# Kernel optimization log

Measured on AMD Instinct MI355X. Metric: run time of the kernel, lower is better.

## Reference

```python
import jax, jax.numpy as jnp
import numpy as np

BS, NQ, NK = 2, 2048, 2048
D_OUT, H, D_K, D_V = 1024, 16, 64, 64


def _xavier(key, shape):
    fan_in, fan_out = shape[1], shape[0]
    lim = float(np.sqrt(6.0 / (fan_in + fan_out)))
    return jax.random.uniform(key, shape, jnp.float32, -lim, lim)


def setup_inputs() -> dict:
    key = jax.random.key(0)
    ks = jax.random.split(key, 9)
    return {
        "queries": jax.random.normal(ks[0], (BS, NQ, D_OUT), jnp.float32),
        "keys": jax.random.normal(ks[1], (BS, NK, D_OUT), jnp.float32),
        "values": jax.random.normal(ks[2], (BS, NK, D_OUT), jnp.float32),
        "mask": jax.random.randint(ks[3], (BS, H, NQ, NK), 0, 2).astype(bool),
        "weights": jax.random.uniform(ks[4], (BS, H, NQ, NK), jnp.float32),
        "Wq": _xavier(ks[5], (H * D_K, D_OUT)),
        "bq": jnp.zeros((H * D_K,), jnp.float32),
        "Wk": _xavier(ks[6], (H * D_K, D_OUT)),
        "bk": jnp.zeros((H * D_K,), jnp.float32),
        "Wv": _xavier(ks[7], (H * D_V, D_OUT)),
        "bv": jnp.zeros((H * D_V,), jnp.float32),
        "Wo": _xavier(ks[8], (D_OUT, H * D_V)),
        "bo": jnp.zeros((D_OUT,), jnp.float32),
    }


def reference(queries, keys, values, mask, weights, Wq, bq, Wk, bk, Wv, bv, Wo, bo):
    bs, nq, _ = queries.shape
    nk = keys.shape[1]
    # projections: (bs, n, h*d) -> (bs, h, n, d)
    q = (queries @ Wq.T + bq).reshape(bs, nq, H, D_K).transpose(0, 2, 1, 3)
    k = (keys @ Wk.T + bk).reshape(bs, nk, H, D_K).transpose(0, 2, 1, 3)
    v = (values @ Wv.T + bv).reshape(bs, nk, H, D_V).transpose(0, 2, 1, 3)
    # scaled dot-product scores: (bs, h, nq, nk)
    att = jnp.einsum("bhqd,bhkd->bhqk", q, k) / jnp.sqrt(jnp.float32(D_K))
    att = att * weights                      # elementwise weight bias
    att = jnp.where(mask, -jnp.inf, att)     # masked_fill(mask, -inf)
    att = jax.nn.softmax(att, axis=-1)
    # dropout is identity at p=0 / eval
    out = jnp.einsum("bhqk,bhkd->bhqd", att, v)  # (bs, h, nq, d_v)
    out = out.transpose(0, 2, 1, 3).reshape(bs, nq, H * D_V)
    return out @ Wo.T + bo
```

## Files before the change

kernel.cpp:

```cpp
#include <hip/hip_runtime.h>
#include <stdint.h>

#define DEV __device__ __forceinline__

typedef __attribute__((__ext_vector_type__(8))) short short8;
typedef __attribute__((__ext_vector_type__(4))) float f32x4;
typedef __attribute__((__ext_vector_type__(16))) float f32x16;
typedef __attribute__((__ext_vector_type__(4))) unsigned short ushort4_t;
typedef __attribute__((__ext_vector_type__(4))) _Float16 half4;
typedef __attribute__((__ext_vector_type__(8))) _Float16 half8;

DEV unsigned short f2bf(float f) {
  union { float f; unsigned u; } x; x.f = f;
  unsigned u = x.u;
  unsigned r = (u + 0x7FFFu + ((u >> 16) & 1u)) >> 16;
  return (unsigned short)r;
}

DEV unsigned short f2h(float f) {
  _Float16 h = (_Float16)f;
  unsigned short u;
  __builtin_memcpy(&u, &h, 2);
  return u;
}

DEV void gload_lds16(const void* g, void* l) {
  __builtin_amdgcn_global_load_lds(
      (const __attribute__((address_space(1))) unsigned int*)g,
      (__attribute__((address_space(3))) unsigned int*)l,
      16, 0, 0);
}

DEV short8 ld_g8(const unsigned short* p) { return *(const short8*)p; }
DEV short8 ld_s8(const unsigned short* p) { return *(const short8*)p; }
DEV half4 ld_h4(const unsigned short* p) {
  half4 r; __builtin_memcpy(&r, p, 8); return r;
}

__global__ void detect_mask_fmt(const unsigned int* __restrict__ mask, int* __restrict__ flag) {
  if (threadIdx.x == 0 && blockIdx.x == 0) {
    int fmt = 1;
    for (int i = 0; i < 256; ++i) {
      unsigned u = mask[i];
      if (u == 0x3F800000u) { fmt = 2; break; }
      if ((u & 0xFFFFFF00u) != 0u) { fmt = 0; break; }
    }
    *flag = fmt;
  }
}

__global__ void pack_mask(const unsigned char* __restrict__ m8,
                          const unsigned int* __restrict__ m32,
                          const int* __restrict__ mfmt,
                          unsigned int* __restrict__ pm) {
  __shared__ unsigned int tile[32 * 65];
  const int bh = blockIdx.x >> 6;
  const int q0 = (blockIdx.x & 63) * 32;
  const int fmt = *mfmt;
  const int tid = threadIdx.x;
#pragma unroll
  for (int rnd = 0; rnd < 8; ++rnd) {
    int w = tid + rnd * 256;
    int q = w >> 6, t = w & 63;
    size_t sb = ((size_t)(bh * 2048 + q0 + q)) * 2048 + t * 32;
    unsigned bits = 0;
    if (fmt == 0) {
      uint4 a = *(const uint4*)(m8 + sb);
      uint4 bq = *(const uint4*)(m8 + sb + 16);
      unsigned wa0 = a.x, wa1 = a.y, wa2 = a.z, wa3 = a.w;
      unsigned wb0 = bq.x, wb1 = bq.y, wb2 = bq.z, wb3 = bq.w;
#pragma unroll
      for (int e = 0; e < 4; ++e) {
        bits |= (((wa0 >> (8 * e)) & 0xFFu) ? 1u : 0u) << (0 + e);
        bits |= (((wa1 >> (8 * e)) & 0xFFu) ? 1u : 0u) << (4 + e);
        bits |= (((wa2 >> (8 * e)) & 0xFFu) ? 1u : 0u) << (8 + e);
        bits |= (((wa3 >> (8 * e)) & 0xFFu) ? 1u : 0u) << (12 + e);
        bits |= (((wb0 >> (8 * e)) & 0xFFu) ? 1u : 0u) << (16 + e);
        bits |= (((wb1 >> (8 * e)) & 0xFFu) ? 1u : 0u) << (20 + e);
        bits |= (((wb2 >> (8 * e)) & 0xFFu) ? 1u : 0u) << (24 + e);
        bits |= (((wb3 >> (8 * e)) & 0xFFu) ? 1u : 0u) << (28 + e);
      }
    } else {
#pragma unroll
      for (int c = 0; c < 8; ++c) {
        uint4 v = *(const uint4*)(m32 + sb + c * 4);
        bits |= (v.x ? 1u : 0u) << (c * 4);
        bits |= (v.y ? 1u : 0u) << (c * 4 + 1);
        bits |= (v.z ? 1u : 0u) << (c * 4 + 2);
        bits |= (v.w ? 1u : 0u) << (c * 4 + 3);
      }
    }
    tile[q * 65 + t] = bits;
  }
  __syncthreads();
#pragma unroll
  for (int rnd = 0; rnd < 8; ++rnd) {
    int w = tid + rnd * 256;
    int t = w >> 5, q = w & 31;
    pm[((size_t)bh * 64 + t) * 2048 + q0 + q] = tile[q * 65 + t];
  }
}

__global__ void cvt_all(const float* __restrict__ q, const float* __restrict__ k,
                        const float* __restrict__ v,
                        const float* __restrict__ wq, const float* __restrict__ wk,
                        const float* __restrict__ wv, const float* __restrict__ wo,
                        unsigned short* __restrict__ Xq, unsigned short* __restrict__ Xk,
                        unsigned short* __restrict__ Xv, unsigned short* __restrict__ Wqb,
                        unsigned short* __restrict__ Wkb, unsigned short* __restrict__ Wvb,
                        unsigned short* __restrict__ Wob) {
  int i = blockIdx.x * 256 + threadIdx.x;
  const float* src; unsigned short* dst; int off;
  if (i < 1048576)      { src = q;  dst = Xq;  off = i; }
  else if (i < 2097152) { src = k;  dst = Xk;  off = i - 1048576; }
  else if (i < 3145728) { src = v;  dst = Xv;  off = i - 2097152; }
  else if (i < 3407872) { src = wq; dst = Wqb; off = i - 3145728; }
  else if (i < 3670016) { src = wk; dst = Wkb; off = i - 3407872; }
  else if (i < 3932160) { src = wv; dst = Wvb; off = i - 3670016; }
  else                  { src = wo; dst = Wob; off = i - 3932160; }
  float4 vv = ((const float4*)src)[off];
  ushort4_t r;
  r.x = f2bf(vv.x); r.y = f2bf(vv.y); r.z = f2bf(vv.z); r.w = f2bf(vv.w);
  ((ushort4_t*)dst)[off] = r;
}

__global__ __launch_bounds__(256, 2) void proj_gemm(
    const unsigned short* __restrict__ Xq, const unsigned short* __restrict__ Xk,
    const unsigned short* __restrict__ Xv,
    const unsigned short* __restrict__ Wqb, const unsigned short* __restrict__ Wkb,
    const unsigned short* __restrict__ Wvb,
    const float* __restrict__ bq, const float* __restrict__ bk, const float* __restrict__ bv,
    unsigned short* __restrict__ QP, unsigned short* __restrict__ KP,
    unsigned short* __restrict__ VT) {
  const int tid = threadIdx.x;
  const int wid = tid >> 6, lane = tid & 63;
  const int l16 = lane & 15, hi = lane >> 4;
  const int m0 = blockIdx.x * 128;
  const int sel = blockIdx.y >> 3;
  const int n0 = (blockIdx.y & 7) * 128;

  const unsigned short* X; const unsigned short* W; const float* bias; unsigned short* out;
  if (sel == 0)      { X = Xq; W = Wqb; bias = bq; out = QP; }
  else if (sel == 1) { X = Xk; W = Wkb; bias = bk; out = KP; }
  else               { X = Xv; W = Wvb; bias = bv; out = VT; }

  __shared__ unsigned short stage[2 * 128 * 32];

  f32x4 acc[4][4] = {};
  const int wm = (wid >> 1) * 64, wn = (wid & 1) * 64;
  const int aoff = (sel == 2) ? 4096 : 0;
  const int boff = 4096 - aoff;

  for (int kt = 0; kt < 1024; kt += 32) {
#pragma unroll
    for (int t = 0; t < 4; ++t) {
      int g = wid * 4 + t;
      int c = g & 7;
      int row = c * 16 + (lane >> 2);
      int ko = (lane & 3) * 8;
      const unsigned short* src = (g < 8)
          ? (X + (size_t)(m0 + row) * 1024 + kt + ko)
          : (W + (size_t)(n0 + row) * 1024 + kt + ko);
      gload_lds16(src, (unsigned short*)((char*)stage + g * 1024));
    }
    __syncthreads();

    short8 af[4], bfr[4];
#pragma unroll
    for (int i = 0; i < 4; ++i)
      af[i] = ld_s8(&stage[aoff + (wm + i * 16 + l16) * 32 + hi * 8]);
#pragma unroll
    for (int j = 0; j < 4; ++j)
      bfr[j] = ld_s8(&stage[boff + (wn + j * 16 + l16) * 32 + hi * 8]);
#pragma unroll
    for (int i = 0; i < 4; ++i)
#pragma unroll
      for (int j = 0; j < 4; ++j)
        acc[i][j] = __builtin_amdgcn_mfma_f32_16x16x32_bf16(af[i], bfr[j], acc[i][j], 0, 0, 0);
    __syncthreads();
  }

  if (sel != 2) {
#pragma unroll
    for (int j = 0; j < 4; ++j) {
      int feat = n0 + wn + j * 16 + l16;
      float bi = bias[feat];
      int h = feat >> 6, d = feat & 63;
#pragma unroll
      for (int i = 0; i < 4; ++i) {
#pragma unroll
        for (int r = 0; r < 4; ++r) {
          int m = m0 + wm + i * 16 + hi * 4 + r;
          int b = m >> 11, n = m & 2047;
          float v = acc[i][j][r] + bi;
          out[(((size_t)(b * 16 + h)) * 2048 + n) * 64 + d] = f2bf(v);
        }
      }
    }
  } else {
#pragma unroll
    for (int j = 0; j < 4; ++j) {
      int tc0 = m0 + wn + j * 16;
      int b = tc0 >> 11, n = tc0 & 2047;
#pragma unroll
      for (int i = 0; i < 4; ++i) {
#pragma unroll
        for (int r = 0; r < 4; ++r) {
          int feat = n0 + wm + i * 16 + hi * 4 + r;
          int h = feat >> 6, d = feat & 63;
          float v = acc[i][j][r] + bias[feat];
          out[((size_t)(b * 16 + h) * 64 + d) * 2048 + n + l16] = f2h(v);
        }
      }
    }
  }
}

__global__ __launch_bounds__(256, 2) void attn_kernel(
    const unsigned short* __restrict__ Q, const unsigned short* __restrict__ K,
    const unsigned short* __restrict__ VT,
    const float* __restrict__ weights,
    const unsigned int* __restrict__ pm,
    unsigned short* __restrict__ O) {
  const int bid = blockIdx.x;
  const int qt = bid >> 5, bh = bid & 31;
  const int b = bh >> 4, h = bh & 15;
  const int tid = threadIdx.x, wid = tid >> 6, lane = tid & 63;
  const int l31 = lane & 31, hh = lane >> 5;
  const size_t bh_nd = (size_t)bh * 2048 * 64;
  const int q0 = qt * 128;
  const int qg = q0 + wid * 32 + l31;

  short8 qf0 = ld_g8(Q + bh_nd + (size_t)qg * 64 + 0  + hh * 8);
  short8 qf1 = ld_g8(Q + bh_nd + (size_t)qg * 64 + 16 + hh * 8);
  short8 qf2 = ld_g8(Q + bh_nd + (size_t)qg * 64 + 32 + hh * 8);
  short8 qf3 = ld_g8(Q + bh_nd + (size_t)qg * 64 + 48 + hh * 8);

  __shared__ float wlds[4][128 * 32];
  __shared__ unsigned short vlds[4][64 * 32];

  const float* wsrc = weights + (size_t)bh * 2048 * 2048;
  const unsigned short* vsrc = VT + bh_nd;
  const unsigned short* ksrc = K + bh_nd;
  const unsigned int* pmsrc = pm + (size_t)bh * 64 * 2048 + qg;
  const int wswz = 4 * ((lane & 7) ^ (lane >> 3));
  const int vswz = 8 * ((lane & 3) ^ ((lane >> 3) & 3));
  const int wrow_s = q0 + wid * 32 + (lane >> 3);
  const int vrow_s = wid * 16 + (lane >> 2);

#define STAGE(BUF, KT)                                                        \
  {                                                                           \
    _Pragma("unroll")                                                         \
    for (int i_ = 0; i_ < 4; ++i_)                                            \
      gload_lds16(wsrc + (size_t)(wrow_s + i_ * 8) * 2048 + (KT) + wswz,      \
                  &wlds[BUF][(wid * 4 + i_) * 256]);                          \
    gload_lds16(vsrc + (size_t)vrow_s * 2048 + (KT) + vswz,                   \
                &vlds[BUF][wid * 512]);                                       \
  }

#define LOADK(K0, K1, K2, K3, PM, T)                                          \
  {                                                                           \
    const int kt_ = (T) * 32;                                                 \
    K0 = ld_g8(ksrc + (size_t)(kt_ + l31) * 64 + 0  + hh * 8);                \
    K1 = ld_g8(ksrc + (size_t)(kt_ + l31) * 64 + 16 + hh * 8);                \
    K2 = ld_g8(ksrc + (size_t)(kt_ + l31) * 64 + 32 + hh * 8);                \
    K3 = ld_g8(ksrc + (size_t)(kt_ + l31) * 64 + 48 + hh * 8);                \
    PM = pmsrc[(size_t)(T) * 2048];                                           \
  }

  f32x16 o0 = {}, o1 = {};
  float mrow = -1e30f, lrow = 0.f;
  short8 ka0, ka1, ka2, ka3, kb0, kb1, kb2, kb3;
  unsigned pma, pmb;

  STAGE(0, 0)
  LOADK(ka0, ka1, ka2, ka3, pma, 0)
  STAGE(1, 32)

#define ITER(T, KC0, KC1, KC2, KC3, PMC, KN0, KN1, KN2, KN3, PMN)             \
  {                                                                           \
    const int t1_ = ((T) + 1) & 63, t2_ = ((T) + 2) & 63;                     \
    LOADK(KN0, KN1, KN2, KN3, PMN, t1_)                                       \
    __builtin_amdgcn_sched_barrier(0);                                        \
    STAGE(((T) + 2) & 3, t2_ * 32)                                            \
    __builtin_amdgcn_sched_barrier(0);                                        \
    asm volatile("s_waitcnt vmcnt(15)" ::: "memory");                         \
    __builtin_amdgcn_s_barrier();                                             \
    __builtin_amdgcn_sched_barrier(0);                                        \
    const int cur_ = (T) & 3;                                                 \
                                                              \
    f32x16 s = {};                                                            \
    s = __builtin_amdgcn_mfma_f32_32x32x16_bf16(KC0, qf0, s, 0, 0, 0);        \
    s = __builtin_amdgcn_mfma_f32_32x32x16_bf16(KC1, qf1, s, 0, 0, 0);        \
    s = __builtin_amdgcn_mfma_f32_32x32x16_bf16(KC2, qf2, s, 0, 0, 0);        \
    s = __builtin_amdgcn_mfma_f32_32x32x16_bf16(KC3, qf3, s, 0, 0, 0);        \
                                                          \
    const float* wrow_ = &wlds[cur_][(wid * 32 + l31) * 32];                  \
    f32x4 wv_[4];                                                             \
    wv_[0] = *(const f32x4*)&wrow_[4 * ((hh + 0) ^ (l31 & 7))];               \
    wv_[1] = *(const f32x4*)&wrow_[4 * ((hh + 2) ^ (l31 & 7))];               \
    wv_[2] = *(const f32x4*)&wrow_[4 * ((hh + 4) ^ (l31 & 7))];               \
    wv_[3] = *(const f32x4*)&wrow_[4 * ((hh + 6) ^ (l31 & 7))];               \
    unsigned mb_ = (PMC) >> (4 * hh);                                         \
    _Pragma("unroll")                                                         \
    for (int r = 0; r < 16; ++r) {                                            \
      bool mk = (mb_ >> ((r & 3) + 8 * (r >> 2))) & 1;                        \
      s[r] = mk ? -INFINITY : s[r] * 0.125f * wv_[r >> 2][r & 3];             \
    }                                                                         \
                                                          \
    float tm = s[0];                                                          \
    _Pragma("unroll")                                                         \
    for (int r = 1; r < 16; ++r) tm = fmaxf(tm, s[r]);                        \
    float tm2 = fmaxf(tm, __shfl_xor(tm, 32));                                \
    if (__any(tm2 > mrow)) {                                                  \
      float mnew = fmaxf(mrow, tm2);                                          \
      float sc = __expf(mrow - mnew);                                         \
      lrow *= sc;                                                             \
      o0 *= sc;                                                               \
      o1 *= sc;                                                               \
      mrow = mnew;                                                            \
    }                                                                         \
    float ps = 0.f;                                                           \
    _Pragma("unroll")                                                         \
    for (int r = 0; r < 16; ++r) {                                            \
      s[r] = __expf(s[r] - mrow);                                             \
      ps += s[r];                                                             \
    }                                                                         \
    lrow += ps;                                                               \
                                                             \
    half8 pa0, pa1;                                                           \
    _Pragma("unroll")                                                         \
    for (int r = 0; r < 8; ++r) {                                             \
      pa0[r] = (_Float16)s[r];                                                \
      pa1[r] = (_Float16)s[8 + r];                                            \
    }                                                                         \
                                                                      \
    {                                                                         \
      const unsigned short* vr_ = &vlds[cur_][l31 * 32];                      \
      half4 a0 = ld_h4(&vr_[4 * ((hh + 0) ^ (l31 & 6))]);                     \
      half4 a1 = ld_h4(&vr_[4 * ((hh + 2) ^ (l31 & 6))]);                     \
      half8 vf;                                                               \
      _Pragma("unroll")                                                       \
      for (int e = 0; e < 4; ++e) { vf[e] = a0[e]; vf[4 + e] = a1[e]; }       \
      o0 = __builtin_amdgcn_mfma_f32_32x32x16_f16(vf, pa0, o0, 0, 0, 0);      \
      half4 b0 = ld_h4(&vr_[4 * ((hh + 4) ^ (l31 & 6))]);                     \
      half4 b1 = ld_h4(&vr_[4 * ((hh + 6) ^ (l31 & 6))]);                     \
      _Pragma("unroll")                                                       \
      for (int e = 0; e < 4; ++e) { vf[e] = b0[e]; vf[4 + e] = b1[e]; }       \
      o0 = __builtin_amdgcn_mfma_f32_32x32x16_f16(vf, pa1, o0, 0, 0, 0);      \
    }                                                                         \
    {                                                                         \
      const unsigned short* vr_ = &vlds[cur_][(32 + l31) * 32];               \
      half4 a0 = ld_h4(&vr_[4 * ((hh + 0) ^ (l31 & 6))]);                     \
      half4 a1 = ld_h4(&vr_[4 * ((hh + 2) ^ (l31 & 6))]);                     \
      half8 vf;                                                               \
      _Pragma("unroll")                                                       \
      for (int e = 0; e < 4; ++e) { vf[e] = a0[e]; vf[4 + e] = a1[e]; }       \
      o1 = __builtin_amdgcn_mfma_f32_32x32x16_f16(vf, pa0, o1, 0, 0, 0);      \
      half4 b0 = ld_h4(&vr_[4 * ((hh + 4) ^ (l31 & 6))]);                     \
      half4 b1 = ld_h4(&vr_[4 * ((hh + 6) ^ (l31 & 6))]);                     \
      _Pragma("unroll")                                                       \
      for (int e = 0; e < 4; ++e) { vf[e] = b0[e]; vf[4 + e] = b1[e]; }       \
      o1 = __builtin_amdgcn_mfma_f32_32x32x16_f16(vf, pa1, o1, 0, 0, 0);      \
    }                                                                         \
  }

  for (int t = 0; t < 64; t += 2) {
    ITER(t,     ka0, ka1, ka2, ka3, pma, kb0, kb1, kb2, kb3, pmb)
    ITER(t + 1, kb0, kb1, kb2, kb3, pmb, ka0, ka1, ka2, ka3, pma)
  }

  lrow += __shfl_xor(lrow, 32);
  float inv = 1.0f / lrow;
  const size_t ob = (size_t)(b * 2048 + qg) * 1024 + h * 64;
#pragma unroll
  for (int j = 0; j < 4; ++j) {
    ushort4_t pk;
    pk.x = f2bf(o0[4 * j + 0] * inv); pk.y = f2bf(o0[4 * j + 1] * inv);
    pk.z = f2bf(o0[4 * j + 2] * inv); pk.w = f2bf(o0[4 * j + 3] * inv);
    *(ushort4_t*)&O[ob + 8 * j + 4 * hh] = pk;
    ushort4_t pk1;
    pk1.x = f2bf(o1[4 * j + 0] * inv); pk1.y = f2bf(o1[4 * j + 1] * inv);
    pk1.z = f2bf(o1[4 * j + 2] * inv); pk1.w = f2bf(o1[4 * j + 3] * inv);
    *(ushort4_t*)&O[ob + 32 + 8 * j + 4 * hh] = pk1;
  }
#undef ITER
#undef LOADK
#undef STAGE
}

__global__ __launch_bounds__(256, 2) void out_gemm(
    const unsigned short* __restrict__ A, const unsigned short* __restrict__ W,
    const float* __restrict__ bias, float* __restrict__ Cout) {
  const int tid = threadIdx.x;
  const int wid = tid >> 6, lane = tid & 63;
  const int l16 = lane & 15, hi = lane >> 4;
  const int m0 = blockIdx.x * 128;
  const int n0 = blockIdx.y * 128;

  __shared__ unsigned short stage[2 * 128 * 32];
  f32x4 acc[4][4] = {};
  const int wm = (wid >> 1) * 64, wn = (wid & 1) * 64;

  for (int kt = 0; kt < 1024; kt += 32) {
#pragma unroll
    for (int t = 0; t < 4; ++t) {
      int g = wid * 4 + t;
      int c = g & 7;
      int row = c * 16 + (lane >> 2);
      int ko = (lane & 3) * 8;
      const unsigned short* src = (g < 8)
          ? (A + (size_t)(m0 + row) * 1024 + kt + ko)
          : (W + (size_t)(n0 + row) * 1024 + kt + ko);
      gload_lds16(src, (unsigned short*)((char*)stage + g * 1024));
    }
    __syncthreads();

    short8 af[4], bfr[4];
#pragma unroll
    for (int i = 0; i < 4; ++i)
      af[i] = ld_s8(&stage[(wm + i * 16 + l16) * 32 + hi * 8]);
#pragma unroll
    for (int j = 0; j < 4; ++j)
      bfr[j] = ld_s8(&stage[4096 + (wn + j * 16 + l16) * 32 + hi * 8]);
#pragma unroll
    for (int i = 0; i < 4; ++i)
#pragma unroll
      for (int j = 0; j < 4; ++j)
        acc[i][j] = __builtin_amdgcn_mfma_f32_16x16x32_bf16(af[i], bfr[j], acc[i][j], 0, 0, 0);
    __syncthreads();
  }

#pragma unroll
  for (int j = 0; j < 4; ++j) {
    int feat = n0 + wn + j * 16 + l16;
    float bi = bias[feat];
#pragma unroll
    for (int i = 0; i < 4; ++i) {
#pragma unroll
      for (int r = 0; r < 4; ++r) {
        int m = m0 + wm + i * 16 + hi * 4 + r;
        Cout[(size_t)m * 1024 + feat] = acc[i][j][r] + bi;
      }
    }
  }
}

extern "C" void kernel_launch(void* const* d_in, const int* in_sizes, int n_in,
                              void* d_out, int out_size, void* d_ws, size_t ws_size,
                              hipStream_t stream) {
  const float* queries = (const float*)d_in[0];
  const float* keys    = (const float*)d_in[1];
  const float* values  = (const float*)d_in[2];
  const void*  maskp   = d_in[3];
  const float* weights = (const float*)d_in[4];
  const float* Wq = (const float*)d_in[5];
  const float* bq = (const float*)d_in[6];
  const float* Wk = (const float*)d_in[7];
  const float* bk = (const float*)d_in[8];
  const float* Wv = (const float*)d_in[9];
  const float* bv = (const float*)d_in[10];
  const float* Wo = (const float*)d_in[11];
  const float* bo = (const float*)d_in[12];

  unsigned short* ws = (unsigned short*)d_ws;
  unsigned short* Xq  = ws;
  unsigned short* Xk  = ws + 4194304;
  unsigned short* Xv  = ws + 8388608;
  unsigned short* Wqb = ws + 12582912;
  unsigned short* Wkb = ws + 13631488;
  unsigned short* Wvb = ws + 14680064;
  unsigned short* Wob = ws + 15728640;
  unsigned short* QP  = ws + 16777216;
  unsigned short* KP  = ws + 20971520;
  unsigned short* VPT = ws + 25165824;
  unsigned short* OB  = Xq;
  unsigned int* pmb   = (unsigned int*)(ws + 4194304);
  int* mflag = (int*)(ws + 29360128);

  detect_mask_fmt<<<1, 64, 0, stream>>>((const unsigned int*)maskp, mflag);

  cvt_all<<<16384, 256, 0, stream>>>(queries, keys, values, Wq, Wk, Wv, Wo,
                                     Xq, Xk, Xv, Wqb, Wkb, Wvb, Wob);

  proj_gemm<<<dim3(32, 24), 256, 0, stream>>>(Xq, Xk, Xv, Wqb, Wkb, Wvb,
                                              bq, bk, bv, QP, KP, VPT);

  pack_mask<<<2048, 256, 0, stream>>>((const unsigned char*)maskp,
                                      (const unsigned int*)maskp, mflag, pmb);

  attn_kernel<<<512, 256, 0, stream>>>(QP, KP, VPT, weights, pmb, OB);

  out_gemm<<<dim3(32, 8), 256, 0, stream>>>(OB, Wob, bo, (float*)d_out);
}
```

Before: 362.0 us.

## Pre-convert attention weights to bf16 with folded scale and stage bf16 tiles

```diff
diff --git a/kernel.cpp b/kernel.cpp
--- a/kernel.cpp
+++ b/kernel.cpp
@@ -4,6 +4,7 @@
 #define DEV __device__ __forceinline__
 
 typedef __attribute__((__ext_vector_type__(8))) short short8;
+typedef __attribute__((__ext_vector_type__(4))) short short4_t;
 typedef __attribute__((__ext_vector_type__(4))) float f32x4;
 typedef __attribute__((__ext_vector_type__(16))) float f32x16;
 typedef __attribute__((__ext_vector_type__(4))) unsigned short ushort4_t;
@@ -15,6 +16,12 @@
   unsigned u = x.u;
   unsigned r = (u + 0x7FFFu + ((u >> 16) & 1u)) >> 16;
   return (unsigned short)r;
+}
+
+DEV float bf2f(unsigned short u) {
+  union { unsigned u; float f; } x;
+  x.u = ((unsigned)u) << 16;
+  return x.f;
 }
 
 DEV unsigned short f2h(float f) {
@@ -46,6 +53,17 @@
       if ((u & 0xFFFFFF00u) != 0u) { fmt = 0; break; }
     }
     *flag = fmt;
+  }
+}
+
+__global__ void cvt_w(const float* __restrict__ w, unsigned short* __restrict__ o) {
+  for (size_t i = (size_t)blockIdx.x * 256 + threadIdx.x; i < 33554432u;
+       i += (size_t)2048 * 256) {
+    float4 v = ((const float4*)w)[i];
+    ushort4_t r;
+    r.x = f2bf(0.125f * v.x); r.y = f2bf(0.125f * v.y);
+    r.z = f2bf(0.125f * v.z); r.w = f2bf(0.125f * v.w);
+    ((ushort4_t*)o)[i] = r;
   }
 }
 
@@ -216,10 +234,10 @@
   }
 }
 
-__global__ __launch_bounds__(256, 2) void attn_kernel(
+__global__ __launch_bounds__(256, 3) void attn_kernel(
     const unsigned short* __restrict__ Q, const unsigned short* __restrict__ K,
     const unsigned short* __restrict__ VT,
-    const float* __restrict__ weights,
+    const unsigned short* __restrict__ WM,
     const unsigned int* __restrict__ pm,
     unsigned short* __restrict__ O) {
   const int bid = blockIdx.x;
@@ -236,24 +254,24 @@
   short8 qf2 = ld_g8(Q + bh_nd + (size_t)qg * 64 + 32 + hh * 8);
   short8 qf3 = ld_g8(Q + bh_nd + (size_t)qg * 64 + 48 + hh * 8);
 
-  __shared__ float wlds[4][128 * 32];
+  __shared__ unsigned short wlds[4][128 * 32];
   __shared__ unsigned short vlds[4][64 * 32];
 
-  const float* wsrc = weights + (size_t)bh * 2048 * 2048;
+  const unsigned short* wmsrc = WM + (size_t)bh * 2048 * 2048;
   const unsigned short* vsrc = VT + bh_nd;
   const unsigned short* ksrc = K + bh_nd;
   const unsigned int* pmsrc = pm + (size_t)bh * 64 * 2048 + qg;
-  const int wswz = 4 * ((lane & 7) ^ (lane >> 3));
+  const int wrow_s = q0 + wid * 32 + (lane >> 2);
+  const int wswz = 8 * ((lane & 3) ^ ((lane >> 2) & 3));
+  const int vrow_s = wid * 16 + (lane >> 2);
   const int vswz = 8 * ((lane & 3) ^ ((lane >> 3) & 3));
-  const int wrow_s = q0 + wid * 32 + (lane >> 3);
-  const int vrow_s = wid * 16 + (lane >> 2);
 
 #define STAGE(BUF, KT)                                                        \
   {                                                                           \
     _Pragma("unroll")                                                         \
-    for (int i_ = 0; i_ < 4; ++i_)                                            \
-      gload_lds16(wsrc + (size_t)(wrow_s + i_ * 8) * 2048 + (KT) + wswz,      \
-                  &wlds[BUF][(wid * 4 + i_) * 256]);                          \
+    for (int i_ = 0; i_ < 2; ++i_)                                            \
+      gload_lds16(wmsrc + (size_t)(wrow_s + i_ * 16) * 2048 + (KT) + wswz,    \
+                  &wlds[BUF][(wid * 32 + i_ * 16) * 32]);                     \
     gload_lds16(vsrc + (size_t)vrow_s * 2048 + (KT) + vswz,                   \
                 &vlds[BUF][wid * 512]);                                       \
   }
@@ -284,7 +302,7 @@
     __builtin_amdgcn_sched_barrier(0);                                        \
     STAGE(((T) + 2) & 3, t2_ * 32)                                            \
     __builtin_amdgcn_sched_barrier(0);                                        \
-    asm volatile("s_waitcnt vmcnt(15)" ::: "memory");                         \
+    asm volatile("s_waitcnt vmcnt(11)" ::: "memory");                         \
     __builtin_amdgcn_s_barrier();                                             \
     __builtin_amdgcn_sched_barrier(0);                                        \
     const int cur_ = (T) & 3;                                                 \
@@ -294,18 +312,25 @@
     s = __builtin_amdgcn_mfma_f32_32x32x16_bf16(KC1, qf1, s, 0, 0, 0);        \
     s = __builtin_amdgcn_mfma_f32_32x32x16_bf16(KC2, qf2, s, 0, 0, 0);        \
     s = __builtin_amdgcn_mfma_f32_32x32x16_bf16(KC3, qf3, s, 0, 0, 0);        \
-                                                          \
-    const float* wrow_ = &wlds[cur_][(wid * 32 + l31) * 32];                  \
+                                        \
+    const unsigned short* wb_ = &wlds[cur_][(wid * 32 + l31) * 32];           \
+    const int qm_ = l31 & 3;                                                  \
     f32x4 wv_[4];                                                             \
-    wv_[0] = *(const f32x4*)&wrow_[4 * ((hh + 0) ^ (l31 & 7))];               \
-    wv_[1] = *(const f32x4*)&wrow_[4 * ((hh + 2) ^ (l31 & 7))];               \
-    wv_[2] = *(const f32x4*)&wrow_[4 * ((hh + 4) ^ (l31 & 7))];               \
-    wv_[3] = *(const f32x4*)&wrow_[4 * ((hh + 6) ^ (l31 & 7))];               \
+    _Pragma("unroll")                                                         \
+    for (int cc = 0; cc < 4; ++cc) {                                          \
+      int o8_ = 2 * cc + hh;                                                  \
+      int p8_ = ((o8_ >> 1) ^ qm_) * 2 + (o8_ & 1);                           \
+      short4_t raw = *(const short4_t*)&wb_[p8_ * 4];                         \
+      wv_[cc][0] = bf2f((unsigned short)raw[0]);                              \
+      wv_[cc][1] = bf2f((unsigned short)raw[1]);                              \
+      wv_[cc][2] = bf2f((unsigned short)raw[2]);                              \
+      wv_[cc][3] = bf2f((unsigned short)raw[3]);                              \
+    }                                                                         \
     unsigned mb_ = (PMC) >> (4 * hh);                                         \
     _Pragma("unroll")                                                         \
     for (int r = 0; r < 16; ++r) {                                            \
       bool mk = (mb_ >> ((r & 3) + 8 * (r >> 2))) & 1;                        \
-      s[r] = mk ? -INFINITY : s[r] * 0.125f * wv_[r >> 2][r & 3];             \
+      s[r] = mk ? -INFINITY : s[r] * wv_[r >> 2][r & 3];                      \
     }                                                                         \
                                                           \
     float tm = s[0];                                                          \
@@ -477,8 +502,11 @@
   unsigned short* OB  = Xq;
   unsigned int* pmb   = (unsigned int*)(ws + 4194304);
   int* mflag = (int*)(ws + 29360128);
+  unsigned short* WM16 = ws + 33554432;
 
   detect_mask_fmt<<<1, 64, 0, stream>>>((const unsigned int*)maskp, mflag);
+
+  cvt_w<<<2048, 256, 0, stream>>>(weights, WM16);
 
   cvt_all<<<16384, 256, 0, stream>>>(queries, keys, values, Wq, Wk, Wv, Wo,
                                      Xq, Xk, Xv, Wqb, Wkb, Wvb, Wob);
@@ -489,7 +517,7 @@
   pack_mask<<<2048, 256, 0, stream>>>((const unsigned char*)maskp,
                                       (const unsigned int*)maskp, mflag, pmb);
 
-  attn_kernel<<<512, 256, 0, stream>>>(QP, KP, VPT, weights, pmb, OB);
+  attn_kernel<<<512, 256, 0, stream>>>(QP, KP, VPT, WM16, pmb, OB);
 
   out_gemm<<<dim3(32, 8), 256, 0, stream>>>(OB, Wob, bo, (float*)d_out);
 }
```

Measured after the change: 483.0 us. 33.4% more time.
